# Kernel tuning notes

Measured on AMD Instinct MI355X. Metric: run time of the kernel, lower is better.

Reference implementation:

```python
import jax, jax.numpy as jnp
import numpy as np

NF = 64
UP = 4
# ktype 's' tap offsets within the 3x3 window
TAPS = ((0, 0), (0, 1), (1, 0), (1, 1))


def setup_inputs() -> dict:
    key = jax.random.key(0)
    ks = jax.random.split(key, 14)
    B, C, H, W = 8, 3, 192, 192
    x = jax.random.normal(ks[0], (B, C, H, W), dtype=jnp.float32)
    def lin(k, fan_in, fan_out):
        s = 1.0 / np.sqrt(fan_in)
        return jax.random.uniform(k, (fan_out, fan_in), jnp.float32, -s, s)
    def bias(k, fan_in, fan_out):
        s = 1.0 / np.sqrt(fan_in)
        return jax.random.uniform(k, (fan_out,), jnp.float32, -s, s)
    inp = {"x": x}
    inp["W1"], inp["b1"] = lin(ks[1], 4, NF), bias(ks[2], 4, NF)
    inp["W2"], inp["b2"] = lin(ks[3], NF, NF), bias(ks[4], NF, NF)
    inp["W3"], inp["b3"] = lin(ks[5], NF, NF), bias(ks[6], NF, NF)
    inp["W4"], inp["b4"] = lin(ks[7], NF, NF), bias(ks[8], NF, NF)
    inp["W5"], inp["b5"] = lin(ks[9], NF, NF), bias(ks[10], NF, NF)
    inp["W6"], inp["b6"] = lin(ks[11], NF, UP * UP), bias(ks[12], NF, UP * UP)
    return inp


def _forward(x, W1, b1, W2, b2, W3, b3, W4, b4, W5, b5, W6, b6):
    B, C, H, W = x.shape
    h, w = H - 2, W - 2
    xi = x.reshape(B * C, H, W)  # each channel processed independently
    taps = jnp.stack([xi[:, di:di + h, dj:dj + w] for di, dj in TAPS], axis=-1)
    # conv1: tiny 4->nf linear, then the outer act() in forward
    f = jax.nn.relu(jnp.einsum('nhwk,fk->nhwf', taps, W1) + b1)
    # conv2..conv5: 1x1 ActConv (conv then ReLU)
    for Wm, bm in ((W2, b2), (W3, b3), (W4, b4), (W5, b5)):
        f = jax.nn.relu(jnp.einsum('nhwf,gf->nhwg', f, Wm) + bm)
    # conv6: 1x1 to upscale^2 channels (no act)
    y = jnp.einsum('nhwf,gf->nhwg', f, W6) + b6  # [N, h, w, r*r]
    # pixel shuffle: out[h*r+i, w*r+j] = y[h, w, i*r+j]
    r = UP
    N = B * C
    y = y.reshape(N, h, w, r, r).transpose(0, 1, 3, 2, 4).reshape(N, h * r, w * r)
    return jnp.tanh(y).reshape(B, C, h * r, w * r)


def reference(x, W1, b1, W2, b2, W3, b3, W4, b4, W5, b5, W6, b6):
    return _forward(x, W1, b1, W2, b2, W3, b3, W4, b4, W5, b5, W6, b6)
```

## Files before the change

### kernel.cpp

```cpp
#include <hip/hip_runtime.h>
#include <cmath>


static constexpr int Hh = 190, Ww = 190, Him = 192, Wim = 192, Nimg = 24;
static constexpr int NPIX = Nimg * Hh * Ww;
static constexpr int NWG  = (NPIX + 511) / 512;

typedef __attribute__((ext_vector_type(8)))  _Float16 half8v;
typedef __attribute__((ext_vector_type(16))) float f32x16;
typedef __attribute__((ext_vector_type(4)))  unsigned int uint4v;

static constexpr int FR_L1  = 0;
static constexpr int FR_L6  = 2;
static constexpr int FR_MID = 6;
static constexpr int BT_BASE = 9728;

__global__ __launch_bounds__(256) void prep_kernel(
    const float* __restrict__ W1, const float* __restrict__ W2,
    const float* __restrict__ W3, const float* __restrict__ W4,
    const float* __restrict__ W5, const float* __restrict__ W6,
    const float* __restrict__ b1, const float* __restrict__ b2,
    const float* __restrict__ b3, const float* __restrict__ b4,
    const float* __restrict__ b5, const float* __restrict__ b6,
    short* __restrict__ ws) {
  float* wsF = (float*)ws;
  int t0 = blockIdx.x * 256 + threadIdx.x;
  int stride = gridDim.x * 256;
  for (int idx = t0; idx < 32 * 512; idx += stride) {
    int j = idx & 7, lane = (idx >> 3) & 63, fi = idx >> 9;
    int ks = fi & 3, mt = (fi >> 2) & 1, L = fi >> 3;
    const float* W = (L == 0) ? W2 : (L == 1) ? W3 : (L == 2) ? W4 : W5;
    int g = mt * 32 + (lane & 31);
    int k = (j & 3) + 8 * (2 * ks + (j >> 2)) + 4 * (lane >> 5);
    _Float16 h = (_Float16)W[g * 64 + k];
    ws[(FR_MID + fi) * 512 + (idx & 511)] = __builtin_bit_cast(short, h);
  }
  for (int idx = t0; idx < 2 * 512; idx += stride) {
    int j = idx & 7, lane = (idx >> 3) & 63, mt = idx >> 9;
    int g = mt * 32 + (lane & 31);
    float w = (j < 4) ? W1[g * 4 + j] : 0.f;
    _Float16 h = (_Float16)w;
    ws[(FR_L1 + mt) * 512 + (idx & 511)] = __builtin_bit_cast(short, h);
  }
  for (int idx = t0; idx < 4 * 512; idx += stride) {
    int j = idx & 7, lane = (idx >> 3) & 63, ks = idx >> 9;
    int g = lane & 31;
    int k = (j & 3) + 8 * (2 * ks + (j >> 2)) + 4 * (lane >> 5);
    float w = (g < 16) ? W6[g * 64 + k] : 0.f;
    _Float16 h = (_Float16)w;
    ws[(FR_L6 + ks) * 512 + (idx & 511)] = __builtin_bit_cast(short, h);
  }
  for (int idx = t0; idx < 256; idx += stride) {
    int r = idx & 15, b5v = (idx >> 4) & 1, mt = (idx >> 5) & 1, L = idx >> 6;
    const float* bb = (L == 0) ? b2 : (L == 1) ? b3 : (L == 2) ? b4 : b5;
    wsF[BT_BASE + idx] = bb[mt * 32 + (r >> 2) * 8 + b5v * 4 + (r & 3)];
  }
  for (int idx = t0; idx < 64; idx += stride) {
    int r = idx & 15, b5v = (idx >> 4) & 1, mt = idx >> 5;
    wsF[BT_BASE + 256 + idx] = b1[mt * 32 + (r >> 2) * 8 + b5v * 4 + (r & 3)];
  }
  for (int idx = t0; idx < 32; idx += stride) {
    int r = idx & 15, b5v = idx >> 4;
    wsF[BT_BASE + 320 + idx] = (r < 8) ? b6[(r >> 2) * 8 + b5v * 4 + (r & 3)] : 0.f;
  }
}


__device__ __forceinline__ unsigned pkrtz(float a, float b) {
  unsigned r;
  asm("v_cvt_pkrtz_f16_f32 %0, %1, %2" : "=v"(r) : "v"(a), "v"(b));
  return r;
}

__device__ __forceinline__ half8v mkfrag(unsigned a0, unsigned a1,
                                         unsigned b0, unsigned b1) {
  uint4v u = {a0, a1, b0, b1};
  return __builtin_bit_cast(half8v, u);
}

__device__ __forceinline__ void epi_tile(const f32x16& acc, half8v (&o)[2]) {
#pragma unroll
  for (int s = 0; s < 2; ++s) {
    unsigned h[4];
#pragma unroll
    for (int d = 0; d < 4; ++d) {
      float v0 = fmaxf(acc[8 * s + 2 * d + 0], 0.f);
      float v1 = fmaxf(acc[8 * s + 2 * d + 1], 0.f);
      h[d] = pkrtz(v0, v1);
    }
    o[s] = mkfrag(h[0], h[1], h[2], h[3]);
  }
}

__device__ __forceinline__ void mid_layer(const short* wlds, const float* bt,
    int Lbase, int lane, int b5,
    half8v (&fo)[2][2][2], half8v (&fn)[2][2][2]) {
#pragma unroll
  for (int mt = 0; mt < 2; ++mt) {
    const short* wb = wlds + (Lbase + mt * 4) * 512 + lane * 8;
    half8v a0 = *(const half8v*)(wb + 0 * 512);
    half8v a1 = *(const half8v*)(wb + 1 * 512);
    half8v a2 = *(const half8v*)(wb + 2 * 512);
    half8v a3 = *(const half8v*)(wb + 3 * 512);
    f32x16 bf = *(const f32x16*)(bt + (mt * 2 + b5) * 16);
#pragma unroll
    for (int nt = 0; nt < 2; ++nt) {
      f32x16 acc;
      acc = __builtin_amdgcn_mfma_f32_32x32x16_f16(a0, fo[0][nt][0], bf, 0, 0, 0);
      acc = __builtin_amdgcn_mfma_f32_32x32x16_f16(a1, fo[0][nt][1], acc, 0, 0, 0);
      acc = __builtin_amdgcn_mfma_f32_32x32x16_f16(a2, fo[1][nt][0], acc, 0, 0, 0);
      acc = __builtin_amdgcn_mfma_f32_32x32x16_f16(a3, fo[1][nt][1], acc, 0, 0, 0);
      epi_tile(acc, fn[mt][nt]);
    }
  }
}

__device__ __forceinline__ float ftanh(float x) {
  float e = __expf(2.0f * x);
  return 1.0f - __fdividef(2.0f, e + 1.0f);
}

__global__ __launch_bounds__(512, 4) void fused_kernel(
    const float* __restrict__ x, const short* __restrict__ ws,
    float* __restrict__ out) {
  __shared__ __align__(16) short wlds[16384];
  __shared__ __align__(16) short wl16[3072];
  __shared__ __align__(64) float blds[352];

  const int lane = threadIdx.x & 63;
  const int wave = threadIdx.x >> 6;
  const int b5 = lane >> 5, lo5 = lane & 31;
  const int wavebase = blockIdx.x * 512 + wave * 64;

  int p = wavebase + lane;
  int pc = p < NPIX ? p : NPIX - 1;
  unsigned jj0 = (unsigned)pc % 190u;
  unsigned r0  = (unsigned)pc / 190u;
  unsigned ii0 = r0 % 190u, nn0 = r0 / 190u;
  const float* xp = x + ((nn0 * 192u + ii0) * 192u + jj0);
  float t0 = xp[0], t1 = xp[1], t2 = xp[192], t3 = xp[193];

  {
    int tid = threadIdx.x;
    const uint4v* src = (const uint4v*)ws;
    if (tid < 384) ((uint4v*)wl16)[tid] = src[tid];
    uint4v* dstM = (uint4v*)wlds;
#pragma unroll
    for (int it = 0; it < 4; ++it)
      dstM[it * 512 + tid] = src[384 + it * 512 + tid];
    const float* wsF = (const float*)ws;
    if (tid < 352) blds[tid] = wsF[BT_BASE + tid];
  }
  __syncthreads();

  half8v fA[2][2][2], fB[2][2][2];

  {
    unsigned th0 = pkrtz(t0, t1), th1 = pkrtz(t2, t3);
    unsigned z = 0u;
    unsigned s0h0 = (b5 == 0) ? th0 : z, s0h1 = (b5 == 0) ? th1 : z;
    unsigned s1h0 = (b5 == 1) ? th0 : z, s1h1 = (b5 == 1) ? th1 : z;
    half8v Bv[2];
    Bv[0] = mkfrag(s0h0, s0h1, s0h0, s0h1);
    Bv[1] = mkfrag(s1h0, s1h1, s1h0, s1h1);
#pragma unroll
    for (int mt = 0; mt < 2; ++mt) {
      f32x16 bf = *(const f32x16*)(blds + 256 + (mt * 2 + b5) * 16);
      half8v a = *(const half8v*)(wl16 + (FR_L1 + mt) * 512 + lane * 8);
#pragma unroll
      for (int nt = 0; nt < 2; ++nt) {
        f32x16 acc = __builtin_amdgcn_mfma_f32_32x32x16_f16(a, Bv[nt], bf, 0, 0, 0);
        epi_tile(acc, fA[mt][nt]);
      }
    }
  }

  mid_layer(wlds, blds + 0 * 64, 0,  lane, b5, fA, fB);
  mid_layer(wlds, blds + 1 * 64, 8,  lane, b5, fB, fA);
  mid_layer(wlds, blds + 2 * 64, 16, lane, b5, fA, fB);
  mid_layer(wlds, blds + 3 * 64, 24, lane, b5, fB, fA);

  {
    f32x16 c6 = *(const f32x16*)(blds + 320 + b5 * 16);
    const short* wb = wl16 + FR_L6 * 512 + lane * 8;
    half8v a0 = *(const half8v*)(wb + 0 * 512);
    half8v a1 = *(const half8v*)(wb + 1 * 512);
    half8v a2 = *(const half8v*)(wb + 2 * 512);
    half8v a3 = *(const half8v*)(wb + 3 * 512);
#pragma unroll
    for (int nt = 0; nt < 2; ++nt) {
      f32x16 a6;
      a6 = __builtin_amdgcn_mfma_f32_32x32x16_f16(a0, fA[0][nt][0], c6, 0, 0, 0);
      a6 = __builtin_amdgcn_mfma_f32_32x32x16_f16(a1, fA[0][nt][1], a6, 0, 0, 0);
      a6 = __builtin_amdgcn_mfma_f32_32x32x16_f16(a2, fA[1][nt][0], a6, 0, 0, 0);
      a6 = __builtin_amdgcn_mfma_f32_32x32x16_f16(a3, fA[1][nt][1], a6, 0, 0, 0);
      int p2 = wavebase + nt * 32 + lo5;
      if (p2 < NPIX) {
        unsigned jj = (unsigned)p2 % 190u;
        unsigned r  = (unsigned)p2 / 190u;
        unsigned ii = r % 190u, nn = r / 190u;
        int base = (int)((nn * 760u + ii * 4u) * 760u + jj * 4u);
        float4 s0, s1;
        s0.x = ftanh(a6[0]); s0.y = ftanh(a6[1]);
        s0.z = ftanh(a6[2]); s0.w = ftanh(a6[3]);
        s1.x = ftanh(a6[4]); s1.y = ftanh(a6[5]);
        s1.z = ftanh(a6[6]); s1.w = ftanh(a6[7]);
        *reinterpret_cast<float4*>(out + base + b5 * 760) = s0;
        *reinterpret_cast<float4*>(out + base + (2 + b5) * 760) = s1;
      }
    }
  }
}

extern "C" void kernel_launch(void* const* d_in, const int* in_sizes, int n_in,
                              void* d_out, int out_size, void* d_ws, size_t ws_size,
                              hipStream_t stream) {
  const float* x  = (const float*)d_in[0];
  const float* W1 = (const float*)d_in[1];
  const float* b1 = (const float*)d_in[2];
  const float* W2 = (const float*)d_in[3];
  const float* b2 = (const float*)d_in[4];
  const float* W3 = (const float*)d_in[5];
  const float* b3 = (const float*)d_in[6];
  const float* W4 = (const float*)d_in[7];
  const float* b4 = (const float*)d_in[8];
  const float* W5 = (const float*)d_in[9];
  const float* b5 = (const float*)d_in[10];
  const float* W6 = (const float*)d_in[11];
  const float* b6 = (const float*)d_in[12];

  hipLaunchKernelGGL(prep_kernel, dim3(64), dim3(256), 0, stream,
                     W1, W2, W3, W4, W5, W6, b1, b2, b3, b4, b5, b6, (short*)d_ws);
  hipLaunchKernelGGL(fused_kernel, dim3(NWG), dim3(512), 0, stream,
                     x, (const short*)d_ws, (float*)d_out);
}
```

Before: 50.39 us.

## Process two pixel batches per wave to interleave independent MFMA chains

Each workgroup now covers 1024 pixels instead of 512, with every wave holding two independent 64-pixel batches. The two MFMA accumulation chains are interleaved so they can hide each other's latency, and each weight fragment loaded from LDS is reused for both batches. The weight LDS fill is also amortized over twice as many pixels. The cost is doubled register pressure for activations and accumulators, which is why launch bounds drop to 2 workgroups per CU, lowering occupancy and halving the grid size.

```diff
diff --git a/kernel.cpp b/kernel.cpp
--- a/kernel.cpp
+++ b/kernel.cpp
@@ -4,7 +4,7 @@
 
 static constexpr int Hh = 190, Ww = 190, Him = 192, Wim = 192, Nimg = 24;
 static constexpr int NPIX = Nimg * Hh * Ww;
-static constexpr int NWG  = (NPIX + 511) / 512;
+static constexpr int NWG  = (NPIX + 1023) / 1024;
 
 typedef __attribute__((ext_vector_type(8)))  _Float16 half8v;
 typedef __attribute__((ext_vector_type(16))) float f32x16;
@@ -92,9 +92,9 @@
   }
 }
 
-__device__ __forceinline__ void mid_layer(const short* wlds, const float* bt,
+__device__ __forceinline__ void mid_layer2(const short* wlds, const float* bt,
     int Lbase, int lane, int b5,
-    half8v (&fo)[2][2][2], half8v (&fn)[2][2][2]) {
+    half8v (&fo)[2][2][2][2], half8v (&fn)[2][2][2][2]) {
 #pragma unroll
   for (int mt = 0; mt < 2; ++mt) {
     const short* wb = wlds + (Lbase + mt * 4) * 512 + lane * 8;
@@ -105,12 +105,17 @@
     f32x16 bf = *(const f32x16*)(bt + (mt * 2 + b5) * 16);
 #pragma unroll
     for (int nt = 0; nt < 2; ++nt) {
-      f32x16 acc;
-      acc = __builtin_amdgcn_mfma_f32_32x32x16_f16(a0, fo[0][nt][0], bf, 0, 0, 0);
-      acc = __builtin_amdgcn_mfma_f32_32x32x16_f16(a1, fo[0][nt][1], acc, 0, 0, 0);
-      acc = __builtin_amdgcn_mfma_f32_32x32x16_f16(a2, fo[1][nt][0], acc, 0, 0, 0);
-      acc = __builtin_amdgcn_mfma_f32_32x32x16_f16(a3, fo[1][nt][1], acc, 0, 0, 0);
-      epi_tile(acc, fn[mt][nt]);
+      f32x16 acc0, acc1;
+      acc0 = __builtin_amdgcn_mfma_f32_32x32x16_f16(a0, fo[0][0][nt][0], bf, 0, 0, 0);
+      acc1 = __builtin_amdgcn_mfma_f32_32x32x16_f16(a0, fo[1][0][nt][0], bf, 0, 0, 0);
+      acc0 = __builtin_amdgcn_mfma_f32_32x32x16_f16(a1, fo[0][0][nt][1], acc0, 0, 0, 0);
+      acc1 = __builtin_amdgcn_mfma_f32_32x32x16_f16(a1, fo[1][0][nt][1], acc1, 0, 0, 0);
+      acc0 = __builtin_amdgcn_mfma_f32_32x32x16_f16(a2, fo[0][1][nt][0], acc0, 0, 0, 0);
+      acc1 = __builtin_amdgcn_mfma_f32_32x32x16_f16(a2, fo[1][1][nt][0], acc1, 0, 0, 0);
+      acc0 = __builtin_amdgcn_mfma_f32_32x32x16_f16(a3, fo[0][1][nt][1], acc0, 0, 0, 0);
+      acc1 = __builtin_amdgcn_mfma_f32_32x32x16_f16(a3, fo[1][1][nt][1], acc1, 0, 0, 0);
+      epi_tile(acc0, fn[0][mt][nt]);
+      epi_tile(acc1, fn[1][mt][nt]);
     }
   }
 }
@@ -120,7 +125,7 @@
   return 1.0f - __fdividef(2.0f, e + 1.0f);
 }
 
-__global__ __launch_bounds__(512, 4) void fused_kernel(
+__global__ __launch_bounds__(512, 2) void fused_kernel(
     const float* __restrict__ x, const short* __restrict__ ws,
     float* __restrict__ out) {
   __shared__ __align__(16) short wlds[16384];
@@ -130,15 +135,19 @@
   const int lane = threadIdx.x & 63;
   const int wave = threadIdx.x >> 6;
   const int b5 = lane >> 5, lo5 = lane & 31;
-  const int wavebase = blockIdx.x * 512 + wave * 64;
-
-  int p = wavebase + lane;
-  int pc = p < NPIX ? p : NPIX - 1;
-  unsigned jj0 = (unsigned)pc % 190u;
-  unsigned r0  = (unsigned)pc / 190u;
-  unsigned ii0 = r0 % 190u, nn0 = r0 / 190u;
-  const float* xp = x + ((nn0 * 192u + ii0) * 192u + jj0);
-  float t0 = xp[0], t1 = xp[1], t2 = xp[192], t3 = xp[193];
+  const int wgbase = blockIdx.x * 1024;
+
+  float t[2][4];
+#pragma unroll
+  for (int b = 0; b < 2; ++b) {
+    int p = wgbase + b * 512 + wave * 64 + lane;
+    int pc = p < NPIX ? p : NPIX - 1;
+    unsigned jj = (unsigned)pc % 190u;
+    unsigned r  = (unsigned)pc / 190u;
+    unsigned ii = r % 190u, nn = r / 190u;
+    const float* xp = x + ((nn * 192u + ii) * 192u + jj);
+    t[b][0] = xp[0]; t[b][1] = xp[1]; t[b][2] = xp[192]; t[b][3] = xp[193];
+  }
 
   {
     int tid = threadIdx.x;
@@ -153,32 +162,37 @@
   }
   __syncthreads();
 
-  half8v fA[2][2][2], fB[2][2][2];
+  half8v fA[2][2][2][2], fB[2][2][2][2];
 
   {
-    unsigned th0 = pkrtz(t0, t1), th1 = pkrtz(t2, t3);
-    unsigned z = 0u;
-    unsigned s0h0 = (b5 == 0) ? th0 : z, s0h1 = (b5 == 0) ? th1 : z;
-    unsigned s1h0 = (b5 == 1) ? th0 : z, s1h1 = (b5 == 1) ? th1 : z;
-    half8v Bv[2];
-    Bv[0] = mkfrag(s0h0, s0h1, s0h0, s0h1);
-    Bv[1] = mkfrag(s1h0, s1h1, s1h0, s1h1);
+    half8v Bv[2][2];
+#pragma unroll
+    for (int b = 0; b < 2; ++b) {
+      unsigned th0 = pkrtz(t[b][0], t[b][1]), th1 = pkrtz(t[b][2], t[b][3]);
+      unsigned z = 0u;
+      unsigned s0h0 = (b5 == 0) ? th0 : z, s0h1 = (b5 == 0) ? th1 : z;
+      unsigned s1h0 = (b5 == 1) ? th0 : z, s1h1 = (b5 == 1) ? th1 : z;
+      Bv[b][0] = mkfrag(s0h0, s0h1, s0h0, s0h1);
+      Bv[b][1] = mkfrag(s1h0, s1h1, s1h0, s1h1);
+    }
 #pragma unroll
     for (int mt = 0; mt < 2; ++mt) {
       f32x16 bf = *(const f32x16*)(blds + 256 + (mt * 2 + b5) * 16);
       half8v a = *(const half8v*)(wl16 + (FR_L1 + mt) * 512 + lane * 8);
 #pragma unroll
       for (int nt = 0; nt < 2; ++nt) {
-        f32x16 acc = __builtin_amdgcn_mfma_f32_32x32x16_f16(a, Bv[nt], bf, 0, 0, 0);
-        epi_tile(acc, fA[mt][nt]);
+        f32x16 acc0 = __builtin_amdgcn_mfma_f32_32x32x16_f16(a, Bv[0][nt], bf, 0, 0, 0);
+        f32x16 acc1 = __builtin_amdgcn_mfma_f32_32x32x16_f16(a, Bv[1][nt], bf, 0, 0, 0);
+        epi_tile(acc0, fA[0][mt][nt]);
+        epi_tile(acc1, fA[1][mt][nt]);
       }
     }
   }
 
-  mid_layer(wlds, blds + 0 * 64, 0,  lane, b5, fA, fB);
-  mid_layer(wlds, blds + 1 * 64, 8,  lane, b5, fB, fA);
-  mid_layer(wlds, blds + 2 * 64, 16, lane, b5, fA, fB);
-  mid_layer(wlds, blds + 3 * 64, 24, lane, b5, fB, fA);
+  mid_layer2(wlds, blds + 0 * 64, 0,  lane, b5, fA, fB);
+  mid_layer2(wlds, blds + 1 * 64, 8,  lane, b5, fB, fA);
+  mid_layer2(wlds, blds + 2 * 64, 16, lane, b5, fA, fB);
+  mid_layer2(wlds, blds + 3 * 64, 24, lane, b5, fB, fA);
 
   {
     f32x16 c6 = *(const f32x16*)(blds + 320 + b5 * 16);
@@ -188,27 +202,29 @@
     half8v a2 = *(const half8v*)(wb + 2 * 512);
     half8v a3 = *(const half8v*)(wb + 3 * 512);
 #pragma unroll
-    for (int nt = 0; nt < 2; ++nt) {
-      f32x16 a6;
-      a6 = __builtin_amdgcn_mfma_f32_32x32x16_f16(a0, fA[0][nt][0], c6, 0, 0, 0);
-      a6 = __builtin_amdgcn_mfma_f32_32x32x16_f16(a1, fA[0][nt][1], a6, 0, 0, 0);
-      a6 = __builtin_amdgcn_mfma_f32_32x32x16_f16(a2, fA[1][nt][0], a6, 0, 0, 0);
-      a6 = __builtin_amdgcn_mfma_f32_32x32x16_f16(a3, fA[1][nt][1], a6, 0, 0, 0);
-      int p2 = wavebase + nt * 32 + lo5;
-      if (p2 < NPIX) {
-        unsigned jj = (unsigned)p2 % 190u;
-        unsigned r  = (unsigned)p2 / 190u;
-        unsigned ii = r % 190u, nn = r / 190u;
-        int base = (int)((nn * 760u + ii * 4u) * 760u + jj * 4u);
-        float4 s0, s1;
-        s0.x = ftanh(a6[0]); s0.y = ftanh(a6[1]);
-        s0.z = ftanh(a6[2]); s0.w = ftanh(a6[3]);
-        s1.x = ftanh(a6[4]); s1.y = ftanh(a6[5]);
-        s1.z = ftanh(a6[6]); s1.w = ftanh(a6[7]);
-        *reinterpret_cast<float4*>(out + base + b5 * 760) = s0;
-        *reinterpret_cast<float4*>(out + base + (2 + b5) * 760) = s1;
+    for (int b = 0; b < 2; ++b)
+#pragma unroll
+      for (int nt = 0; nt < 2; ++nt) {
+        f32x16 a6;
+        a6 = __builtin_amdgcn_mfma_f32_32x32x16_f16(a0, fA[b][0][nt][0], c6, 0, 0, 0);
+        a6 = __builtin_amdgcn_mfma_f32_32x32x16_f16(a1, fA[b][0][nt][1], a6, 0, 0, 0);
+        a6 = __builtin_amdgcn_mfma_f32_32x32x16_f16(a2, fA[b][1][nt][0], a6, 0, 0, 0);
+        a6 = __builtin_amdgcn_mfma_f32_32x32x16_f16(a3, fA[b][1][nt][1], a6, 0, 0, 0);
+        int p2 = wgbase + b * 512 + wave * 64 + nt * 32 + lo5;
+        if (p2 < NPIX) {
+          unsigned jj = (unsigned)p2 % 190u;
+          unsigned r  = (unsigned)p2 / 190u;
+          unsigned ii = r % 190u, nn = r / 190u;
+          int base = (int)((nn * 760u + ii * 4u) * 760u + jj * 4u);
+          float4 s0, s1;
+          s0.x = ftanh(a6[0]); s0.y = ftanh(a6[1]);
+          s0.z = ftanh(a6[2]); s0.w = ftanh(a6[3]);
+          s1.x = ftanh(a6[4]); s1.y = ftanh(a6[5]);
+          s1.z = ftanh(a6[6]); s1.w = ftanh(a6[7]);
+          *reinterpret_cast<float4*>(out + base + b5 * 760) = s0;
+          *reinterpret_cast<float4*>(out + base + (2 + b5) * 760) = s1;
+        }
       }
-    }
   }
 }
 
```

After: 54.66 us. 8.5% more time.

## Fold weight prep into fused kernel and process two chunks per block

Applied to the files above, without the earlier changes.

Removes the separate prep kernel launch: each block now converts and swizzles the fp32 weights and biases into fp16 MFMA fragment layout directly in LDS. To amortize this per-block conversion (scattered global reads, 32 serial iterations), each workgroup now processes two 512-pixel chunks, halving the grid. This trades a launch and workspace round-trip for redundant per-block weight conversion and fewer, longer blocks.

```diff
diff --git a/kernel.cpp b/kernel.cpp
--- a/kernel.cpp
+++ b/kernel.cpp
@@ -4,7 +4,8 @@
 
 static constexpr int Hh = 190, Ww = 190, Him = 192, Wim = 192, Nimg = 24;
 static constexpr int NPIX = Nimg * Hh * Ww;
-static constexpr int NWG  = (NPIX + 511) / 512;
+static constexpr int NCHUNK = (NPIX + 511) / 512;
+static constexpr int NWG = (NCHUNK + 1) / 2;
 
 typedef __attribute__((ext_vector_type(8)))  _Float16 half8v;
 typedef __attribute__((ext_vector_type(16))) float f32x16;
@@ -12,58 +13,6 @@
 
 static constexpr int FR_L1  = 0;
 static constexpr int FR_L6  = 2;
-static constexpr int FR_MID = 6;
-static constexpr int BT_BASE = 9728;
-
-__global__ __launch_bounds__(256) void prep_kernel(
-    const float* __restrict__ W1, const float* __restrict__ W2,
-    const float* __restrict__ W3, const float* __restrict__ W4,
-    const float* __restrict__ W5, const float* __restrict__ W6,
-    const float* __restrict__ b1, const float* __restrict__ b2,
-    const float* __restrict__ b3, const float* __restrict__ b4,
-    const float* __restrict__ b5, const float* __restrict__ b6,
-    short* __restrict__ ws) {
-  float* wsF = (float*)ws;
-  int t0 = blockIdx.x * 256 + threadIdx.x;
-  int stride = gridDim.x * 256;
-  for (int idx = t0; idx < 32 * 512; idx += stride) {
-    int j = idx & 7, lane = (idx >> 3) & 63, fi = idx >> 9;
-    int ks = fi & 3, mt = (fi >> 2) & 1, L = fi >> 3;
-    const float* W = (L == 0) ? W2 : (L == 1) ? W3 : (L == 2) ? W4 : W5;
-    int g = mt * 32 + (lane & 31);
-    int k = (j & 3) + 8 * (2 * ks + (j >> 2)) + 4 * (lane >> 5);
-    _Float16 h = (_Float16)W[g * 64 + k];
-    ws[(FR_MID + fi) * 512 + (idx & 511)] = __builtin_bit_cast(short, h);
-  }
-  for (int idx = t0; idx < 2 * 512; idx += stride) {
-    int j = idx & 7, lane = (idx >> 3) & 63, mt = idx >> 9;
-    int g = mt * 32 + (lane & 31);
-    float w = (j < 4) ? W1[g * 4 + j] : 0.f;
-    _Float16 h = (_Float16)w;
-    ws[(FR_L1 + mt) * 512 + (idx & 511)] = __builtin_bit_cast(short, h);
-  }
-  for (int idx = t0; idx < 4 * 512; idx += stride) {
-    int j = idx & 7, lane = (idx >> 3) & 63, ks = idx >> 9;
-    int g = lane & 31;
-    int k = (j & 3) + 8 * (2 * ks + (j >> 2)) + 4 * (lane >> 5);
-    float w = (g < 16) ? W6[g * 64 + k] : 0.f;
-    _Float16 h = (_Float16)w;
-    ws[(FR_L6 + ks) * 512 + (idx & 511)] = __builtin_bit_cast(short, h);
-  }
-  for (int idx = t0; idx < 256; idx += stride) {
-    int r = idx & 15, b5v = (idx >> 4) & 1, mt = (idx >> 5) & 1, L = idx >> 6;
-    const float* bb = (L == 0) ? b2 : (L == 1) ? b3 : (L == 2) ? b4 : b5;
-    wsF[BT_BASE + idx] = bb[mt * 32 + (r >> 2) * 8 + b5v * 4 + (r & 3)];
-  }
-  for (int idx = t0; idx < 64; idx += stride) {
-    int r = idx & 15, b5v = (idx >> 4) & 1, mt = idx >> 5;
-    wsF[BT_BASE + 256 + idx] = b1[mt * 32 + (r >> 2) * 8 + b5v * 4 + (r & 3)];
-  }
-  for (int idx = t0; idx < 32; idx += stride) {
-    int r = idx & 15, b5v = idx >> 4;
-    wsF[BT_BASE + 320 + idx] = (r < 8) ? b6[(r >> 2) * 8 + b5v * 4 + (r & 3)] : 0.f;
-  }
-}
 
 
 __device__ __forceinline__ unsigned pkrtz(float a, float b) {
@@ -93,7 +42,7 @@
 }
 
 __device__ __forceinline__ void mid_layer(const short* wlds, const float* bt,
-    int Lbase, int lane, int b5,
+    int Lbase, int lane, int hb,
     half8v (&fo)[2][2][2], half8v (&fn)[2][2][2]) {
 #pragma unroll
   for (int mt = 0; mt < 2; ++mt) {
@@ -102,7 +51,7 @@
     half8v a1 = *(const half8v*)(wb + 1 * 512);
     half8v a2 = *(const half8v*)(wb + 2 * 512);
     half8v a3 = *(const half8v*)(wb + 3 * 512);
-    f32x16 bf = *(const f32x16*)(bt + (mt * 2 + b5) * 16);
+    f32x16 bf = *(const f32x16*)(bt + (mt * 2 + hb) * 16);
 #pragma unroll
     for (int nt = 0; nt < 2; ++nt) {
       f32x16 acc;
@@ -121,92 +70,131 @@
 }
 
 __global__ __launch_bounds__(512, 4) void fused_kernel(
-    const float* __restrict__ x, const short* __restrict__ ws,
+    const float* __restrict__ x,
+    const float* __restrict__ W1, const float* __restrict__ W2,
+    const float* __restrict__ W3, const float* __restrict__ W4,
+    const float* __restrict__ W5, const float* __restrict__ W6,
+    const float* __restrict__ b1, const float* __restrict__ b2,
+    const float* __restrict__ b3, const float* __restrict__ b4,
+    const float* __restrict__ b5, const float* __restrict__ b6,
     float* __restrict__ out) {
   __shared__ __align__(16) short wlds[16384];
   __shared__ __align__(16) short wl16[3072];
   __shared__ __align__(64) float blds[352];
 
-  const int lane = threadIdx.x & 63;
-  const int wave = threadIdx.x >> 6;
-  const int b5 = lane >> 5, lo5 = lane & 31;
-  const int wavebase = blockIdx.x * 512 + wave * 64;
-
-  int p = wavebase + lane;
-  int pc = p < NPIX ? p : NPIX - 1;
-  unsigned jj0 = (unsigned)pc % 190u;
-  unsigned r0  = (unsigned)pc / 190u;
-  unsigned ii0 = r0 % 190u, nn0 = r0 / 190u;
-  const float* xp = x + ((nn0 * 192u + ii0) * 192u + jj0);
-  float t0 = xp[0], t1 = xp[1], t2 = xp[192], t3 = xp[193];
+  const int tid = threadIdx.x;
+  const int lane = tid & 63;
+  const int wave = tid >> 6;
+  const int hb = lane >> 5, lo5 = lane & 31;
 
   {
-    int tid = threadIdx.x;
-    const uint4v* src = (const uint4v*)ws;
-    if (tid < 384) ((uint4v*)wl16)[tid] = src[tid];
-    uint4v* dstM = (uint4v*)wlds;
-#pragma unroll
-    for (int it = 0; it < 4; ++it)
-      dstM[it * 512 + tid] = src[384 + it * 512 + tid];
-    const float* wsF = (const float*)ws;
-    if (tid < 352) blds[tid] = wsF[BT_BASE + tid];
+    int j = tid & 7, plane = tid >> 3;
+    int g_lo = plane & 31, hbit = plane >> 5;
+#pragma unroll 1
+    for (int it = 0; it < 32; ++it) {
+      int ks = it & 3, mt = (it >> 2) & 1, L = it >> 3;
+      const float* W = (L == 0) ? W2 : (L == 1) ? W3 : (L == 2) ? W4 : W5;
+      int g = mt * 32 + g_lo;
+      int k = (j & 3) + 8 * (2 * ks + (j >> 2)) + 4 * hbit;
+      _Float16 h = (_Float16)W[g * 64 + k];
+      wlds[it * 512 + tid] = __builtin_bit_cast(short, h);
+    }
+#pragma unroll
+    for (int it = 0; it < 2; ++it) {
+      int g = it * 32 + g_lo;
+      float w = (j < 4) ? W1[g * 4 + j] : 0.f;
+      _Float16 h = (_Float16)w;
+      wl16[(FR_L1 + it) * 512 + tid] = __builtin_bit_cast(short, h);
+    }
+#pragma unroll
+    for (int it = 0; it < 4; ++it) {
+      int k = (j & 3) + 8 * (2 * it + (j >> 2)) + 4 * hbit;
+      float w = (g_lo < 16) ? W6[g_lo * 64 + k] : 0.f;
+      _Float16 h = (_Float16)w;
+      wl16[(FR_L6 + it) * 512 + tid] = __builtin_bit_cast(short, h);
+    }
+    if (tid < 256) {
+      int r = tid & 15, hv = (tid >> 4) & 1, mt = (tid >> 5) & 1, L = tid >> 6;
+      const float* bb = (L == 0) ? b2 : (L == 1) ? b3 : (L == 2) ? b4 : b5;
+      blds[tid] = bb[mt * 32 + (r >> 2) * 8 + hv * 4 + (r & 3)];
+    } else if (tid < 320) {
+      int i2 = tid - 256;
+      int r = i2 & 15, hv = (i2 >> 4) & 1, mt = i2 >> 5;
+      blds[tid] = b1[mt * 32 + (r >> 2) * 8 + hv * 4 + (r & 3)];
+    } else if (tid < 352) {
+      int i2 = tid - 320;
+      int r = i2 & 15, hv = i2 >> 4;
+      blds[tid] = (r < 8) ? b6[(r >> 2) * 8 + hv * 4 + (r & 3)] : 0.f;
+    }
   }
   __syncthreads();
 
-  half8v fA[2][2][2], fB[2][2][2];
-
-  {
-    unsigned th0 = pkrtz(t0, t1), th1 = pkrtz(t2, t3);
-    unsigned z = 0u;
-    unsigned s0h0 = (b5 == 0) ? th0 : z, s0h1 = (b5 == 0) ? th1 : z;
-    unsigned s1h0 = (b5 == 1) ? th0 : z, s1h1 = (b5 == 1) ? th1 : z;
-    half8v Bv[2];
-    Bv[0] = mkfrag(s0h0, s0h1, s0h0, s0h1);
-    Bv[1] = mkfrag(s1h0, s1h1, s1h0, s1h1);
-#pragma unroll
-    for (int mt = 0; mt < 2; ++mt) {
-      f32x16 bf = *(const f32x16*)(blds + 256 + (mt * 2 + b5) * 16);
-      half8v a = *(const half8v*)(wl16 + (FR_L1 + mt) * 512 + lane * 8);
+#pragma unroll
+  for (int c = 0; c < 2; ++c) {
+    const int wavebase = (blockIdx.x * 2 + c) * 512 + wave * 64;
+
+    half8v fA[2][2][2], fB[2][2][2];
+
+    {
+      int p = wavebase + lane;
+      int pc = p < NPIX ? p : NPIX - 1;
+      unsigned jj = (unsigned)pc % 190u;
+      unsigned r  = (unsigned)pc / 190u;
+      unsigned ii = r % 190u, nn = r / 190u;
+      const float* xp = x + ((nn * 192u + ii) * 192u + jj);
+      float t0 = xp[0], t1 = xp[1], t2 = xp[192], t3 = xp[193];
+      unsigned th0 = pkrtz(t0, t1), th1 = pkrtz(t2, t3);
+      unsigned z = 0u;
+      unsigned s0h0 = (hb == 0) ? th0 : z, s0h1 = (hb == 0) ? th1 : z;
+      unsigned s1h0 = (hb == 1) ? th0 : z, s1h1 = (hb == 1) ? th1 : z;
+      half8v Bv[2];
+      Bv[0] = mkfrag(s0h0, s0h1, s0h0, s0h1);
+      Bv[1] = mkfrag(s1h0, s1h1, s1h0, s1h1);
+#pragma unroll
+      for (int mt = 0; mt < 2; ++mt) {
+        f32x16 bf = *(const f32x16*)(blds + 256 + (mt * 2 + hb) * 16);
+        half8v a = *(const half8v*)(wl16 + (FR_L1 + mt) * 512 + lane * 8);
+#pragma unroll
+        for (int nt = 0; nt < 2; ++nt) {
+          f32x16 acc = __builtin_amdgcn_mfma_f32_32x32x16_f16(a, Bv[nt], bf, 0, 0, 0);
+          epi_tile(acc, fA[mt][nt]);
+        }
+      }
+    }
+
+    mid_layer(wlds, blds + 0 * 64, 0,  lane, hb, fA, fB);
+    mid_layer(wlds, blds + 1 * 64, 8,  lane, hb, fB, fA);
+    mid_layer(wlds, blds + 2 * 64, 16, lane, hb, fA, fB);
+    mid_layer(wlds, blds + 3 * 64, 24, lane, hb, fB, fA);
+
+    {
+      f32x16 c6 = *(const f32x16*)(blds + 320 + hb * 16);
+      const short* wb = wl16 + FR_L6 * 512 + lane * 8;
+      half8v a0 = *(const half8v*)(wb + 0 * 512);
+      half8v a1 = *(const half8v*)(wb + 1 * 512);
+      half8v a2 = *(const half8v*)(wb + 2 * 512);
+      half8v a3 = *(const half8v*)(wb + 3 * 512);
 #pragma unroll
       for (int nt = 0; nt < 2; ++nt) {
-        f32x16 acc = __builtin_amdgcn_mfma_f32_32x32x16_f16(a, Bv[nt], bf, 0, 0, 0);
-        epi_tile(acc, fA[mt][nt]);
-      }
-    }
-  }
-
-  mid_layer(wlds, blds + 0 * 64, 0,  lane, b5, fA, fB);
-  mid_layer(wlds, blds + 1 * 64, 8,  lane, b5, fB, fA);
-  mid_layer(wlds, blds + 2 * 64, 16, lane, b5, fA, fB);
-  mid_layer(wlds, blds + 3 * 64, 24, lane, b5, fB, fA);
-
-  {
-    f32x16 c6 = *(const f32x16*)(blds + 320 + b5 * 16);
-    const short* wb = wl16 + FR_L6 * 512 + lane * 8;
-    half8v a0 = *(const half8v*)(wb + 0 * 512);
-    half8v a1 = *(const half8v*)(wb + 1 * 512);
-    half8v a2 = *(const half8v*)(wb + 2 * 512);
-    half8v a3 = *(const half8v*)(wb + 3 * 512);
-#pragma unroll
-    for (int nt = 0; nt < 2; ++nt) {
-      f32x16 a6;
-      a6 = __builtin_amdgcn_mfma_f32_32x32x16_f16(a0, fA[0][nt][0], c6, 0, 0, 0);
-      a6 = __builtin_amdgcn_mfma_f32_32x32x16_f16(a1, fA[0][nt][1], a6, 0, 0, 0);
-      a6 = __builtin_amdgcn_mfma_f32_32x32x16_f16(a2, fA[1][nt][0], a6, 0, 0, 0);
-      a6 = __builtin_amdgcn_mfma_f32_32x32x16_f16(a3, fA[1][nt][1], a6, 0, 0, 0);
-      int p2 = wavebase + nt * 32 + lo5;
-      if (p2 < NPIX) {
-        unsigned jj = (unsigned)p2 % 190u;
-        unsigned r  = (unsigned)p2 / 190u;
-        unsigned ii = r % 190u, nn = r / 190u;
-        int base = (int)((nn * 760u + ii * 4u) * 760u + jj * 4u);
-        float4 s0, s1;
-        s0.x = ftanh(a6[0]); s0.y = ftanh(a6[1]);
-        s0.z = ftanh(a6[2]); s0.w = ftanh(a6[3]);
-        s1.x = ftanh(a6[4]); s1.y = ftanh(a6[5]);
-        s1.z = ftanh(a6[6]); s1.w = ftanh(a6[7]);
-        *reinterpret_cast<float4*>(out + base + b5 * 760) = s0;
-        *reinterpret_cast<float4*>(out + base + (2 + b5) * 760) = s1;
+        f32x16 a6;
+        a6 = __builtin_amdgcn_mfma_f32_32x32x16_f16(a0, fA[0][nt][0], c6, 0, 0, 0);
+        a6 = __builtin_amdgcn_mfma_f32_32x32x16_f16(a1, fA[0][nt][1], a6, 0, 0, 0);
+        a6 = __builtin_amdgcn_mfma_f32_32x32x16_f16(a2, fA[1][nt][0], a6, 0, 0, 0);
+        a6 = __builtin_amdgcn_mfma_f32_32x32x16_f16(a3, fA[1][nt][1], a6, 0, 0, 0);
+        int p2 = wavebase + nt * 32 + lo5;
+        if (p2 < NPIX) {
+          unsigned jj = (unsigned)p2 % 190u;
+          unsigned r  = (unsigned)p2 / 190u;
+          unsigned ii = r % 190u, nn = r / 190u;
+          int base = (int)((nn * 760u + ii * 4u) * 760u + jj * 4u);
+          float4 s0, s1;
+          s0.x = ftanh(a6[0]); s0.y = ftanh(a6[1]);
+          s0.z = ftanh(a6[2]); s0.w = ftanh(a6[3]);
+          s1.x = ftanh(a6[4]); s1.y = ftanh(a6[5]);
+          s1.z = ftanh(a6[6]); s1.w = ftanh(a6[7]);
+          *reinterpret_cast<float4*>(out + base + hb * 760) = s0;
+          *reinterpret_cast<float4*>(out + base + (2 + hb) * 760) = s1;
+        }
       }
     }
   }
@@ -229,8 +217,7 @@
   const float* W6 = (const float*)d_in[11];
   const float* b6 = (const float*)d_in[12];
 
-  hipLaunchKernelGGL(prep_kernel, dim3(64), dim3(256), 0, stream,
-                     W1, W2, W3, W4, W5, W6, b1, b2, b3, b4, b5, b6, (short*)d_ws);
   hipLaunchKernelGGL(fused_kernel, dim3(NWG), dim3(512), 0, stream,
-                     x, (const short*)d_ws, (float*)d_out);
-}
+                     x, W1, W2, W3, W4, W5, W6,
+                     b1, b2, b3, b4, b5, b6, (float*)d_out);
+}
```

Measured after the change: 56.46 us. +12.0%, slower.
